# Kernel optimization log

Measured on AMD Instinct MI355X. Metric: run time of the kernel, lower is better.

The kernel has to match this reference:

```python
import jax, jax.numpy as jnp
import numpy as np

N, E, IN, H, ED, G, OUT = 50000, 800000, 128, 256, 32, 500, 16
LN_EPS = 1e-5
BN_EPS = 1e-5


def _w(key, shape, scale=0.05):
    return scale * jax.random.normal(key, shape, dtype=jnp.float32)


def setup_inputs() -> dict:
    key = jax.random.key(0)
    ks = iter(jax.random.split(key, 64))
    inp = {
        'x': jax.random.normal(next(ks), (N, IN), jnp.float32),
        'edge_index': jax.random.randint(next(ks), (2, E), 0, N, jnp.int64),
        'edge_attr': jax.random.normal(next(ks), (E, ED), jnp.float32),
        'batch': jnp.sort(jax.random.randint(next(ks), (N,), 0, G, jnp.int64)),
    }
    def conv_params(pfx, din):
        return {
            pfx + '_Wq': _w(next(ks), (din, H)), pfx + '_bq': jnp.zeros((H,), jnp.float32),
            pfx + '_Wk': _w(next(ks), (din, H)), pfx + '_bk': jnp.zeros((H,), jnp.float32),
            pfx + '_Wv': _w(next(ks), (din, H)), pfx + '_bv': jnp.zeros((H,), jnp.float32),
            pfx + '_We': _w(next(ks), (ED, H)),
            pfx + '_Ws': _w(next(ks), (din, H)), pfx + '_bs': jnp.zeros((H,), jnp.float32),
        }
    inp.update(conv_params('conv1', IN))
    inp.update({'ln1_g': jnp.ones((H,), jnp.float32), 'ln1_b': jnp.zeros((H,), jnp.float32)})
    inp.update(conv_params('conv2', H))
    inp.update({'ln2_g': jnp.ones((H,), jnp.float32), 'ln2_b': jnp.zeros((H,), jnp.float32)})
    for pfx in ('gin1', 'gin2'):
        inp.update({
            pfx + '_W1': _w(next(ks), (H, H)), pfx + '_b1': jnp.zeros((H,), jnp.float32),
            pfx + '_bng': jnp.ones((H,), jnp.float32), pfx + '_bnb': jnp.zeros((H,), jnp.float32),
            pfx + '_W2': _w(next(ks), (H, H)), pfx + '_b2': jnp.zeros((H,), jnp.float32),
        })
    inp.update({'lin_W': _w(next(ks), (H, H)), 'lin_b': jnp.zeros((H,), jnp.float32),
                'clf_W': _w(next(ks), (H, OUT)), 'clf_b': jnp.zeros((OUT,), jnp.float32)})
    return inp


def transformer_conv(x, src, dst, ea, Wq, bq, Wk, bk, Wv, bv, We, Ws, bs):
    # PyG TransformerConv, heads=1, edge_dim set, root_weight=True, beta=False
    h = Wq.shape[1]
    q = x @ Wq + bq                      # [N,H]
    e = ea @ We                          # [E,H]
    ke = (x @ Wk + bk)[src] + e          # [E,H]
    ve = (x @ Wv + bv)[src] + e          # [E,H]
    score = jnp.sum(q[dst] * ke, axis=-1) / jnp.sqrt(jnp.float32(h))  # [E]
    m = jax.ops.segment_max(score, dst, num_segments=N)
    ex = jnp.exp(score - m[dst])
    denom = jax.ops.segment_sum(ex, dst, num_segments=N)
    alpha = ex / (denom[dst] + 1e-16)
    out = jax.ops.segment_sum(alpha[:, None] * ve, dst, num_segments=N)
    return out + x @ Ws + bs


def layer_norm(x, g, b):
    mu = jnp.mean(x, axis=-1, keepdims=True)
    var = jnp.var(x, axis=-1, keepdims=True)
    return (x - mu) * jax.lax.rsqrt(var + LN_EPS) * g + b


def gin_conv(x, src, dst, W1, b1, bng, bnb, W2, b2):
    # GINConv(eps=0): mlp(x + sum_{j in N(i)} x_j); MLP = Linear-BN-ReLU-Linear
    agg = jax.ops.segment_sum(x[src], dst, num_segments=N)
    h = x + agg
    y = h @ W1 + b1
    mu = jnp.mean(y, axis=0)
    var = jnp.var(y, axis=0)
    y = (y - mu) * jax.lax.rsqrt(var + BN_EPS) * bng + bnb
    y = jax.nn.relu(y)
    return y @ W2 + b2


def reference(x, edge_index, edge_attr, batch,
              conv1_Wq, conv1_bq, conv1_Wk, conv1_bk, conv1_Wv, conv1_bv, conv1_We, conv1_Ws, conv1_bs,
              ln1_g, ln1_b,
              conv2_Wq, conv2_bq, conv2_Wk, conv2_bk, conv2_Wv, conv2_bv, conv2_We, conv2_Ws, conv2_bs,
              ln2_g, ln2_b,
              gin1_W1, gin1_b1, gin1_bng, gin1_bnb, gin1_W2, gin1_b2,
              gin2_W1, gin2_b1, gin2_bng, gin2_bnb, gin2_W2, gin2_b2,
              lin_W, lin_b, clf_W, clf_b):
    src, dst = edge_index[0], edge_index[1]
    # NodeEncoder (dropout inactive in eval)
    h = transformer_conv(x, src, dst, edge_attr, conv1_Wq, conv1_bq, conv1_Wk, conv1_bk,
                         conv1_Wv, conv1_bv, conv1_We, conv1_Ws, conv1_bs)
    h = layer_norm(jax.nn.leaky_relu(h), ln1_g, ln1_b)
    h = transformer_conv(h, src, dst, edge_attr, conv2_Wq, conv2_bq, conv2_Wk, conv2_bk,
                         conv2_Wv, conv2_bv, conv2_We, conv2_Ws, conv2_bs)
    h = layer_norm(jax.nn.leaky_relu(h), ln2_g, ln2_b)
    # GIN_Net, max_depth=2: conv -> relu -> conv
    h = gin_conv(h, src, dst, gin1_W1, gin1_b1, gin1_bng, gin1_bnb, gin1_W2, gin1_b2)
    h = jax.nn.relu(h)
    h = gin_conv(h, src, dst, gin2_W1, gin2_b1, gin2_bng, gin2_bnb, gin2_W2, gin2_b2)
    # global_add_pool + MLP head
    pooled = jax.ops.segment_sum(h, batch, num_segments=G)   # [G,H]
    z = jax.nn.relu(pooled @ lin_W + lin_b)
    return z @ clf_W + clf_b                                 # [G,OUT]
```

## Files before the change

kernel.cpp:

```cpp
#include <hip/hip_runtime.h>
#include <math.h>

#define NN 50000
#define NE 800000
#define DIN 128
#define DH 256
#define DED 32
#define NG 500
#define DOUT 16
#define SCAN_T 256

typedef __bf16 bf16_t;
typedef __bf16 bf16x4 __attribute__((ext_vector_type(4)));
typedef __bf16 bf16x8 __attribute__((ext_vector_type(8)));
typedef float f32x4 __attribute__((ext_vector_type(4)));

__device__ __forceinline__ void async_copy16(const bf16_t* g, bf16_t* l) {
  __builtin_amdgcn_global_load_lds(
      (const __attribute__((address_space(1))) void*)g,
      (__attribute__((address_space(3))) void*)l, 16, 0, 0);
}

__global__ void fill_i32(int* __restrict__ p, int v, int n) {
  int i = blockIdx.x * 256 + threadIdx.x;
  if (i < n) p[i] = v;
}
__global__ void cast_bf16x8_k(const float* __restrict__ in, bf16_t* __restrict__ o, long n8) {
  long i = (long)blockIdx.x * 256 + threadIdx.x;
  if (i >= n8) return;
  const float* sp = &in[i * 8];
  bf16x8 r;
#pragma unroll
  for (int j = 0; j < 8; ++j) r[j] = (bf16_t)sp[j];
  *(bf16x8*)&o[i * 8] = r;
}

__global__ void count_k(const int* __restrict__ dst, int* __restrict__ deg) {
  int e = blockIdx.x * 256 + threadIdx.x;
  if (e < NE) atomicAdd(&deg[dst[e]], 1);
}
__global__ void scan1(const int* __restrict__ deg, int* __restrict__ rowptr,
                      int* __restrict__ bsum, int n) {
  __shared__ int s[SCAN_T];
  int t = threadIdx.x, i = blockIdx.x * SCAN_T + t;
  int v = (i < n) ? deg[i] : 0;
  s[t] = v; __syncthreads();
  for (int off = 1; off < SCAN_T; off <<= 1) {
    int add = (t >= off) ? s[t - off] : 0;
    __syncthreads(); s[t] += add; __syncthreads();
  }
  if (i < n) rowptr[i + 1] = s[t];
  if (t == SCAN_T - 1) bsum[blockIdx.x] = s[t];
}
__global__ void scan2(const int* __restrict__ bsum, int* __restrict__ boff, int nb) {
  __shared__ int s[SCAN_T];
  int t = threadIdx.x;
  int v = (t < nb) ? bsum[t] : 0;
  s[t] = v; __syncthreads();
  for (int off = 1; off < SCAN_T; off <<= 1) {
    int add = (t >= off) ? s[t - off] : 0;
    __syncthreads(); s[t] += add; __syncthreads();
  }
  boff[t] = s[t] - v;
}
__global__ void scan3(int* __restrict__ rowptr, const int* __restrict__ boff, int n) {
  int i = blockIdx.x * 256 + threadIdx.x;
  if (i < n) rowptr[i + 1] += boff[i >> 8];
  if (i == 0) rowptr[0] = 0;
}
__global__ void scatter_k(const int* __restrict__ dst, const int* __restrict__ src,
                          const int* __restrict__ rowptr, int* __restrict__ cursor,
                          int* __restrict__ esrc, int* __restrict__ epos) {
  int e = blockIdx.x * 256 + threadIdx.x;
  if (e < NE) {
    int d = dst[e];
    int pos = rowptr[d] + atomicAdd(&cursor[d], 1);
    esrc[pos] = src[e];
    epos[e] = pos;
  }
}
__global__ void permute_ea(const int* __restrict__ epos, const float* __restrict__ ea,
                           bf16_t* __restrict__ eac) {
  long t = (long)blockIdx.x * 256 + threadIdx.x;
  if (t >= (long)NE * 4) return;
  int e = (int)(t >> 2), c8 = ((int)t & 3) * 8;
  int pos = epos[e];
  const float* sp = &ea[(size_t)e * DED + c8];
  bf16x8 o;
#pragma unroll
  for (int j = 0; j < 8; ++j) o[j] = (bf16_t)sp[j];
  *(bf16x8*)&eac[(size_t)pos * DED + c8] = o;
}

struct PackEnt { const float* src; bf16_t* dst; int K; int N; };
struct PackArgs { PackEnt e[16]; };
__global__ void pack_all(PackArgs pa) {
  PackEnt en = pa.e[blockIdx.y];
  int i = blockIdx.x * 256 + threadIdx.x;
  if (i >= en.K * en.N) return;
  int el = i & 511, f = i >> 9;
  int ntiles = en.N >> 4;
  int ks = f / ntiles, t = f - ks * ntiles;
  int lane = el >> 3, j = el & 7;
  int k = ks * 32 + (lane >> 4) * 8 + j;
  int n = t * 16 + (lane & 15);
  en.dst[i] = (bf16_t)en.src[(size_t)k * en.N + n];
}

__global__ void wqe_k(const float* __restrict__ Wq, const float* __restrict__ We,
                      const float* __restrict__ bq, float* __restrict__ Wqe,
                      float* __restrict__ bqe, int din) {
  int idx = blockIdx.x * 256 + threadIdx.x;
  if (idx < din * 32) {
    int d = idx >> 5, j = idx & 31;
    float s = 0.f;
    for (int h = 0; h < DH; ++h) s += Wq[(size_t)d * DH + h] * We[(size_t)j * DH + h];
    Wqe[idx] = s;
  }
  if (idx < 32) {
    float s = 0.f;
    for (int h = 0; h < DH; ++h) s += bq[h] * We[(size_t)idx * DH + h];
    bqe[idx] = s;
  }
}

template<int NT, int RT>
__device__ __forceinline__ void gemm_body(
    const bf16_t* __restrict__ Ab, const bf16_t* __restrict__ Wp,
    const float* __restrict__ bias, float* __restrict__ Cf, bf16_t* __restrict__ Cb,
    int M, int K, int relu, int rstride, int bx,
    float* __restrict__ psum, float* __restrict__ psq)
{
  __shared__ bf16_t Atile[RT * 2048];
  __shared__ bf16_t Btile[NT * 512];
  int tid = threadIdx.x;
  int lane = tid & 63, wv = tid >> 6;
  int base = bx * (RT * 64);
  f32x4 acc[RT][NT];
#pragma unroll
  for (int rt = 0; rt < RT; ++rt)
#pragma unroll
    for (int t = 0; t < NT; ++t) acc[rt][t] = (f32x4){0.f, 0.f, 0.f, 0.f};
  int arow = wv * (16 * RT) + (lane & 15);
  int aq = (lane >> 4) * 8;
  int nk = K >> 5;
  const int ACH = RT * 256;
  const int NCH = ACH + NT * 64;
  for (int ks = 0; ks < nk; ++ks) {
    __syncthreads();
    for (int c = tid; c < NCH; c += 256) {
      if (c < ACH) {
        int r = c >> 2, q = c & 3;
        async_copy16(Ab + (size_t)(base + r) * K + ks * 32 + q * 8, &Atile[c * 8]);
      } else {
        int cb = c - ACH;
        async_copy16(Wp + (size_t)ks * NT * 512 + cb * 8, &Btile[cb * 8]);
      }
    }
    __syncthreads();
    bf16x8 a[RT];
#pragma unroll
    for (int rt = 0; rt < RT; ++rt)
      a[rt] = *(const bf16x8*)&Atile[(arow + rt * 16) * 32 + aq];
#pragma unroll
    for (int t = 0; t < NT; ++t) {
      bf16x8 b = *(const bf16x8*)&Btile[t * 512 + lane * 8];
#pragma unroll
      for (int rt = 0; rt < RT; ++rt)
        acc[rt][t] = __builtin_amdgcn_mfma_f32_16x16x32_bf16(a[rt], b, acc[rt][t], 0, 0, 0);
    }
  }
  int col_l = lane & 15;
#pragma unroll
  for (int rt = 0; rt < RT; ++rt) {
    int rbase = base + wv * (16 * RT) + rt * 16 + (lane >> 4) * 4;
#pragma unroll
    for (int t = 0; t < NT; ++t) {
      int col = t * 16 + col_l;
      float bv = bias ? bias[col] : 0.f;
#pragma unroll
      for (int r = 0; r < 4; ++r) {
        int row = rbase + r;
        if (row >= M) continue;
        float vv = acc[rt][t][r] + bv;
        if (relu) vv = fmaxf(vv, 0.f);
        if (Cf) Cf[(size_t)row * rstride + col] = vv;
        if (Cb) Cb[(size_t)row * rstride + col] = (bf16_t)vv;
      }
    }
  }
  if (psum) {
#pragma unroll
    for (int t = 0; t < NT; ++t) {
      float sc = 0.f, sq = 0.f;
      float bv = bias[t * 16 + col_l];
#pragma unroll
      for (int rt = 0; rt < RT; ++rt) {
        int rbase = base + wv * (16 * RT) + rt * 16 + (lane >> 4) * 4;
#pragma unroll
        for (int r = 0; r < 4; ++r) {
          if (rbase + r >= M) continue;
          float vv = acc[rt][t][r] + bv;
          sc += vv; sq += vv * vv;
        }
      }
      sc += __shfl_xor(sc, 16, 64); sc += __shfl_xor(sc, 32, 64);
      sq += __shfl_xor(sq, 16, 64); sq += __shfl_xor(sq, 32, 64);
      if (lane < 16) {
        int col = t * 16 + lane;
        atomicAdd(&psum[wv * DH + col], sc);
        atomicAdd(&psq[wv * DH + col], sq);
      }
    }
  }
}

template<int NT>
__global__ __launch_bounds__(256, 3) void gemm_r1(
    const bf16_t* __restrict__ Ab, const bf16_t* __restrict__ Wp,
    const float* __restrict__ bias, float* __restrict__ Cf, bf16_t* __restrict__ Cb,
    int M, int K, int relu, int rstride, float* psum, float* psq)
{
  gemm_body<NT, 1>(Ab, Wp, bias, Cf, Cb, M, K, relu, rstride, blockIdx.x, psum, psq);
}

struct QkvsArgs { const bf16_t* w[4]; const float* bias[4]; bf16_t* outp[4]; };
__global__ __launch_bounds__(256, 3) void gemm_qkvs(
    const bf16_t* __restrict__ Ab, QkvsArgs qa, int M, int K)
{
  int which = blockIdx.y;
  gemm_body<16, 2>(Ab, qa.w[which], qa.bias[which], nullptr, qa.outp[which], M, K, 0, 1024,
                   blockIdx.x, nullptr, nullptr);
}

__global__ __launch_bounds__(256, 3) void gemm_e2n_ln(
    const bf16_t* __restrict__ Ab, const bf16_t* __restrict__ Wp,
    const bf16_t* __restrict__ AGG, const bf16_t* __restrict__ qkvs,
    const float* __restrict__ g, const float* __restrict__ b,
    bf16_t* __restrict__ out, int M)
{
  __shared__ bf16_t Atile[2048];
  __shared__ bf16_t Btile[16 * 512];
  int tid = threadIdx.x;
  int lane = tid & 63, wv = tid >> 6;
  int base = blockIdx.x * 64;
  for (int c = tid; c < 256 + 1024; c += 256) {
    if (c < 256) {
      int r = c >> 2, q2 = c & 3;
      async_copy16(Ab + (size_t)(base + r) * 32 + q2 * 8, &Atile[c * 8]);
    } else {
      int cb = c - 256;
      async_copy16(Wp + cb * 8, &Btile[cb * 8]);
    }
  }
  __syncthreads();
  bf16x8 a0 = *(const bf16x8*)&Atile[(wv * 16 + (lane & 15)) * 32 + (lane >> 4) * 8];
  f32x4 acc[16];
#pragma unroll
  for (int t = 0; t < 16; ++t) {
    bf16x8 bfr = *(const bf16x8*)&Btile[t * 512 + lane * 8];
    acc[t] = __builtin_amdgcn_mfma_f32_16x16x32_bf16(a0, bfr, (f32x4){0.f,0.f,0.f,0.f}, 0, 0, 0);
  }
  int col_l = lane & 15;
  int rbase = base + wv * 16 + (lane >> 4) * 4;
#pragma unroll
  for (int t = 0; t < 16; ++t) {
    int col = t * 16 + col_l;
#pragma unroll
    for (int r = 0; r < 4; ++r) {
      int row = rbase + r;
      float ag = 0.f, sv = 0.f;
      if (row < M) {
        ag = (float)AGG[(size_t)row * DH + col];
        sv = (float)qkvs[(size_t)row * 1024 + 768 + col];
      }
      float t1 = acc[t][r] + ag + sv;
      acc[t][r] = (t1 > 0.f) ? t1 : 0.01f * t1;
    }
  }
  float mu[4], rstd[4];
#pragma unroll
  for (int r = 0; r < 4; ++r) {
    float sum = 0.f, sq = 0.f;
#pragma unroll
    for (int t = 0; t < 16; ++t) { sum += acc[t][r]; sq += acc[t][r] * acc[t][r]; }
#pragma unroll
    for (int off = 1; off < 16; off <<= 1) {
      sum += __shfl_xor(sum, off, 16);
      sq  += __shfl_xor(sq, off, 16);
    }
    mu[r] = sum * (1.f / DH);
    float var = sq * (1.f / DH) - mu[r] * mu[r];
    rstd[r] = rsqrtf(var + 1e-5f);
  }
#pragma unroll
  for (int t = 0; t < 16; ++t) {
    int col = t * 16 + col_l;
    float gc = g[col], bc = b[col];
#pragma unroll
    for (int r = 0; r < 4; ++r) {
      int row = rbase + r;
      if (row < M)
        out[(size_t)row * DH + col] = (bf16_t)((acc[t][r] - mu[r]) * rstd[r] * gc + bc);
    }
  }
}

__global__ __launch_bounds__(256) void conv_edge_fused(
    const int* __restrict__ rowptr, const int* __restrict__ esrc,
    const bf16_t* __restrict__ qkvs, const bf16_t* __restrict__ eac,
    const float* __restrict__ QEf,
    bf16_t* __restrict__ AGGn, bf16_t* __restrict__ EAn)
{
  int l = threadIdx.x & 31;
  int half = (threadIdx.x >> 5) & 1;
  int n = blockIdx.x * 4 + (threadIdx.x >> 6);
  if (n >= NN) return;
  float q[8];
  {
    bf16x8 t = *(const bf16x8*)&qkvs[(size_t)n * 1024 + l * 8];
#pragma unroll
    for (int j = 0; j < 8; ++j) q[j] = (float)t[j];
  }
  float qe[8];
#pragma unroll
  for (int j = 0; j < 8; ++j) qe[j] = 0.f;
  if (l < 4) {
    const float* p = &QEf[(size_t)n * DED + l * 8];
#pragma unroll
    for (int j = 0; j < 8; ++j) qe[j] = p[j];
  }
  float s = 0.f;
  float acc[8], eacc[8];
#pragma unroll
  for (int j = 0; j < 8; ++j) { acc[j] = 0.f; eacc[j] = 0.f; }
  int i0 = rowptr[n], i1 = rowptr[n + 1];
  for (int wb = i0; wb < i1; wb += 32) {
    int wcnt = min(32, i1 - wb);
    int widx = (l < wcnt) ? esrc[wb + l] : 0;
    int e = 0;
    for (; e + 8 <= wcnt; e += 8) {
      int s1 = __shfl(widx, e + half, 32);
      int s2 = __shfl(widx, e + 2 + half, 32);
      int s3 = __shfl(widx, e + 4 + half, 32);
      int s4 = __shfl(widx, e + 6 + half, 32);
      const bf16_t* b1 = &qkvs[(size_t)s1 * 1024 + 256 + l * 8];
      const bf16_t* b2 = &qkvs[(size_t)s2 * 1024 + 256 + l * 8];
      const bf16_t* b3 = &qkvs[(size_t)s3 * 1024 + 256 + l * 8];
      const bf16_t* b4 = &qkvs[(size_t)s4 * 1024 + 256 + l * 8];
      bf16x8 k1 = *(const bf16x8*)b1;
      bf16x8 k2 = *(const bf16x8*)b2;
      bf16x8 k3 = *(const bf16x8*)b3;
      bf16x8 k4 = *(const bf16x8*)b4;
      bf16x8 v1 = *(const bf16x8*)(b1 + 256);
      bf16x8 v2 = *(const bf16x8*)(b2 + 256);
      bf16x8 v3 = *(const bf16x8*)(b3 + 256);
      bf16x8 v4 = *(const bf16x8*)(b4 + 256);
      bf16x8 t1 = {}, t2 = {}, t3 = {}, t4 = {};
      if (l < 4) {
        const bf16_t* ep = &eac[(size_t)(wb + e + half) * DED + l * 8];
        t1 = *(const bf16x8*)ep;
        t2 = *(const bf16x8*)(ep + 2 * DED);
        t3 = *(const bf16x8*)(ep + 4 * DED);
        t4 = *(const bf16x8*)(ep + 6 * DED);
      }
      float p1 = 0.f, p2 = 0.f, p3 = 0.f, p4 = 0.f;
#pragma unroll
      for (int j = 0; j < 8; ++j) {
        p1 = fmaf(q[j], (float)k1[j], p1);
        p2 = fmaf(q[j], (float)k2[j], p2);
        p3 = fmaf(q[j], (float)k3[j], p3);
        p4 = fmaf(q[j], (float)k4[j], p4);
      }
#pragma unroll
      for (int j = 0; j < 8; ++j) {
        p1 = fmaf(qe[j], (float)t1[j], p1);
        p2 = fmaf(qe[j], (float)t2[j], p2);
        p3 = fmaf(qe[j], (float)t3[j], p3);
        p4 = fmaf(qe[j], (float)t4[j], p4);
      }
#pragma unroll
      for (int off = 16; off > 0; off >>= 1) {
        p1 += __shfl_xor(p1, off, 32);
        p2 += __shfl_xor(p2, off, 32);
        p3 += __shfl_xor(p3, off, 32);
        p4 += __shfl_xor(p4, off, 32);
      }
      float ex1 = __expf(p1 * 0.0625f);
      float ex2 = __expf(p2 * 0.0625f);
      float ex3 = __expf(p3 * 0.0625f);
      float ex4 = __expf(p4 * 0.0625f);
      s += (ex1 + ex2) + (ex3 + ex4);
#pragma unroll
      for (int j = 0; j < 8; ++j) {
        acc[j] = fmaf(ex1, (float)v1[j], acc[j]);
        acc[j] = fmaf(ex2, (float)v2[j], acc[j]);
        acc[j] = fmaf(ex3, (float)v3[j], acc[j]);
        acc[j] = fmaf(ex4, (float)v4[j], acc[j]);
      }
#pragma unroll
      for (int j = 0; j < 8; ++j) {
        eacc[j] = fmaf(ex1, (float)t1[j], eacc[j]);
        eacc[j] = fmaf(ex2, (float)t2[j], eacc[j]);
        eacc[j] = fmaf(ex3, (float)t3[j], eacc[j]);
        eacc[j] = fmaf(ex4, (float)t4[j], eacc[j]);
      }
    }
    for (; e < wcnt; e += 2) {
      int eh = e + half;
      bool act = eh < wcnt;
      int s1 = __shfl(widx, act ? eh : e, 32);
      const bf16_t* b1 = &qkvs[(size_t)s1 * 1024 + 256 + l * 8];
      bf16x8 k1 = *(const bf16x8*)b1;
      bf16x8 v1 = *(const bf16x8*)(b1 + 256);
      bf16x8 t1 = {};
      if (act && l < 4) t1 = *(const bf16x8*)&eac[(size_t)(wb + eh) * DED + l * 8];
      float p1 = 0.f;
#pragma unroll
      for (int j = 0; j < 8; ++j) p1 = fmaf(q[j], (float)k1[j], p1);
#pragma unroll
      for (int j = 0; j < 8; ++j) p1 = fmaf(qe[j], (float)t1[j], p1);
#pragma unroll
      for (int off = 16; off > 0; off >>= 1) p1 += __shfl_xor(p1, off, 32);
      float ex1 = act ? __expf(p1 * 0.0625f) : 0.f;
      s += ex1;
#pragma unroll
      for (int j = 0; j < 8; ++j) acc[j] = fmaf(ex1, (float)v1[j], acc[j]);
#pragma unroll
      for (int j = 0; j < 8; ++j) eacc[j] = fmaf(ex1, (float)t1[j], eacc[j]);
    }
  }
  s += __shfl_xor(s, 32, 64);
#pragma unroll
  for (int j = 0; j < 8; ++j) acc[j] += __shfl_xor(acc[j], 32, 64);
#pragma unroll
  for (int j = 0; j < 8; ++j) eacc[j] += __shfl_xor(eacc[j], 32, 64);
  float inv = 1.f / (s + 1e-16f);
  if (half == 0) {
    bf16x8 o;
#pragma unroll
    for (int j = 0; j < 8; ++j) o[j] = (bf16_t)(acc[j] * inv);
    *(bf16x8*)&AGGn[(size_t)n * DH + l * 8] = o;
    if (l < 4) {
      bf16x8 eo;
#pragma unroll
      for (int j = 0; j < 8; ++j) eo[j] = (bf16_t)(eacc[j] * inv);
      *(bf16x8*)&EAn[(size_t)n * DED + l * 8] = eo;
    }
  }
}

__global__ __launch_bounds__(256) void gin_gather(
    const int* __restrict__ rowptr, const int* __restrict__ esrc,
    const bf16_t* __restrict__ h, bf16_t* __restrict__ out)
{
  int l = threadIdx.x & 31;
  int half = (threadIdx.x >> 5) & 1;
  int n = blockIdx.x * 4 + (threadIdx.x >> 6);
  if (n >= NN) return;
  size_t co = (size_t)n * DH + l * 8;
  float acc[8];
  {
    bf16x8 hv = *(const bf16x8*)&h[co];
    float w0 = (half == 0) ? 1.f : 0.f;
#pragma unroll
    for (int j = 0; j < 8; ++j) acc[j] = w0 * (float)hv[j];
  }
  int i0 = rowptr[n], i1 = rowptr[n + 1];
  for (int wb = i0; wb < i1; wb += 32) {
    int wcnt = min(32, i1 - wb);
    int widx = (l < wcnt) ? esrc[wb + l] : 0;
    int e = 0;
    for (; e + 8 <= wcnt; e += 8) {
      int s1 = __shfl(widx, e + half, 32);
      int s2 = __shfl(widx, e + 2 + half, 32);
      int s3 = __shfl(widx, e + 4 + half, 32);
      int s4 = __shfl(widx, e + 6 + half, 32);
      bf16x8 t1 = *(const bf16x8*)&h[(size_t)s1 * DH + l * 8];
      bf16x8 t2 = *(const bf16x8*)&h[(size_t)s2 * DH + l * 8];
      bf16x8 t3 = *(const bf16x8*)&h[(size_t)s3 * DH + l * 8];
      bf16x8 t4 = *(const bf16x8*)&h[(size_t)s4 * DH + l * 8];
#pragma unroll
      for (int j = 0; j < 8; ++j)
        acc[j] += ((float)t1[j] + (float)t2[j]) + ((float)t3[j] + (float)t4[j]);
    }
    for (; e < wcnt; e += 2) {
      int eh = e + half;
      bool act = eh < wcnt;
      int s1 = __shfl(widx, act ? eh : e, 32);
      bf16x8 t1 = *(const bf16x8*)&h[(size_t)s1 * DH + l * 8];
      float w = act ? 1.f : 0.f;
#pragma unroll
      for (int j = 0; j < 8; ++j) acc[j] += w * (float)t1[j];
    }
  }
#pragma unroll
  for (int j = 0; j < 8; ++j) acc[j] += __shfl_xor(acc[j], 32, 64);
  if (half == 0) {
    bf16x8 o;
#pragma unroll
    for (int j = 0; j < 8; ++j) o[j] = (bf16_t)acc[j];
    *(bf16x8*)&out[co] = o;
  }
}

__global__ void bn_final_na(const float* __restrict__ psum, const float* __restrict__ psq,
                            const float* __restrict__ bng, const float* __restrict__ bnb,
                            float* __restrict__ scale, float* __restrict__ shift) {
  int c = threadIdx.x;
  float s = 0.f, ss = 0.f;
  for (int b = 0; b < 4; ++b) { s += psum[b * DH + c]; ss += psq[b * DH + c]; }
  float mu = s * (1.f / NN);
  float var = ss * (1.f / NN) - mu * mu;
  float rstd = rsqrtf(var + 1e-5f);
  float sc = bng[c] * rstd;
  scale[c] = sc;
  shift[c] = bnb[c] - mu * sc;
}
__global__ void bn_apply_relu8(const bf16_t* __restrict__ y, const float* __restrict__ scale,
                               const float* __restrict__ shift, bf16_t* __restrict__ o, int n8) {
  int i = blockIdx.x * 256 + threadIdx.x;
  if (i >= n8) return;
  bf16x8 v = *(const bf16x8*)&y[(size_t)i * 8];
  int c = (i * 8) & (DH - 1);
  bf16x8 r;
#pragma unroll
  for (int j = 0; j < 8; ++j)
    r[j] = (bf16_t)fmaxf((float)v[j] * scale[c + j] + shift[c + j], 0.f);
  *(bf16x8*)&o[(size_t)i * 8] = r;
}

__global__ __launch_bounds__(256) void pool_sorted(
    const int* __restrict__ batch, const bf16_t* __restrict__ h, float* __restrict__ pooled)
{
  __shared__ int s0, s1;
  int g = blockIdx.x;
  if (threadIdx.x == 0) {
    int lo = 0, hi = NN;
    while (lo < hi) { int mid = (lo + hi) >> 1; if (batch[mid] < g) lo = mid + 1; else hi = mid; }
    s0 = lo;
  }
  if (threadIdx.x == 1) {
    int lo = 0, hi = NN;
    while (lo < hi) { int mid = (lo + hi) >> 1; if (batch[mid] < g + 1) lo = mid + 1; else hi = mid; }
    s1 = lo;
  }
  __syncthreads();
  int c = threadIdx.x;
  float acc = 0.f;
  for (int r = s0; r < s1; ++r) acc += (float)h[(size_t)r * DH + c];
  pooled[(size_t)g * DH + c] = acc;
}

__global__ __launch_bounds__(256) void gemm_bias_act(
    const float* __restrict__ A, const float* __restrict__ Wm,
    const float* __restrict__ bias, float* __restrict__ C,
    int M, int K, int Ncol, int act)
{
  __shared__ __align__(16) float As[16][68];
  __shared__ __align__(16) float Bs[16][68];
  int tid = threadIdx.x;
  int tx = tid & 15, ty = tid >> 4;
  int row0 = blockIdx.y * 64 + ty * 4;
  int col0 = blockIdx.x * 64 + tx * 4;
  float acc[4][4] = {{0.f}};
  for (int k0 = 0; k0 < K; k0 += 16) {
#pragma unroll
    for (int l = 0; l < 4; ++l) {
      int e = tid + l * 256;
      int r = e >> 4, kk = e & 15;
      int gr = blockIdx.y * 64 + r;
      As[kk][r] = (gr < M) ? A[(size_t)gr * K + k0 + kk] : 0.f;
    }
#pragma unroll
    for (int l = 0; l < 4; ++l) {
      int e = tid + l * 256;
      int kk = e >> 6, c = e & 63;
      int gc = blockIdx.x * 64 + c;
      Bs[kk][c] = (gc < Ncol) ? Wm[(size_t)(k0 + kk) * Ncol + gc] : 0.f;
    }
    __syncthreads();
#pragma unroll
    for (int kk = 0; kk < 16; ++kk) {
      float4 a4 = *(const float4*)&As[kk][ty * 4];
      float4 b4 = *(const float4*)&Bs[kk][tx * 4];
      float a[4] = {a4.x, a4.y, a4.z, a4.w};
      float b[4] = {b4.x, b4.y, b4.z, b4.w};
#pragma unroll
      for (int i = 0; i < 4; ++i)
#pragma unroll
        for (int j = 0; j < 4; ++j)
          acc[i][j] = fmaf(a[i], b[j], acc[i][j]);
    }
    __syncthreads();
  }
#pragma unroll
  for (int i = 0; i < 4; ++i) {
    int r = row0 + i;
    if (r >= M) continue;
#pragma unroll
    for (int j = 0; j < 4; ++j) {
      int c = col0 + j;
      if (c >= Ncol) continue;
      float val = acc[i][j];
      if (bias) val += bias[c];
      if (act == 1) val = fmaxf(val, 0.f);
      C[(size_t)r * Ncol + c] = val;
    }
  }
}

static inline void launch_filli(hipStream_t st, int* p, int v, long n) {
  fill_i32<<<dim3((unsigned)((n + 255) / 256)), dim3(256), 0, st>>>(p, v, (int)n);
}

extern "C" void kernel_launch(void* const* d_in, const int* in_sizes, int n_in,
                              void* d_out, int out_size, void* d_ws, size_t ws_size,
                              hipStream_t stream) {
  const float* x  = (const float*)d_in[0];
  const int* ei   = (const int*)d_in[1];
  const float* ea = (const float*)d_in[2];
  const int* batch = (const int*)d_in[3];
  const int* src = ei;
  const int* dst = ei + NE;

  const float* c1[9]; for (int i = 0; i < 9; ++i) c1[i] = (const float*)d_in[4 + i];
  const float* ln1g = (const float*)d_in[13]; const float* ln1b = (const float*)d_in[14];
  const float* c2[9]; for (int i = 0; i < 9; ++i) c2[i] = (const float*)d_in[15 + i];
  const float* ln2g = (const float*)d_in[24]; const float* ln2b = (const float*)d_in[25];
  const float* g1[6]; for (int i = 0; i < 6; ++i) g1[i] = (const float*)d_in[26 + i];
  const float* g2[6]; for (int i = 0; i < 6; ++i) g2[i] = (const float*)d_in[32 + i];
  const float* linW = (const float*)d_in[38]; const float* linb = (const float*)d_in[39];
  const float* clfW = (const float*)d_in[40]; const float* clfb = (const float*)d_in[41];
  float* out = (float*)d_out;

  size_t off = 0;
  auto alloc = [&](size_t bytes) -> void* {
    void* r = (char*)d_ws + off;
    off += (bytes + 255) & ~(size_t)255;
    return r;
  };
  int* deg    = (int*)alloc(NN * 4);
  int* cursor = (int*)alloc(NN * 4);
  int* rowptr = (int*)alloc((NN + 1) * 4);
  int* esrc   = (int*)alloc((size_t)NE * 4);
  int* epos   = (int*)alloc((size_t)NE * 4);
  int* bsum   = (int*)alloc(1024);
  int* boff   = (int*)alloc(1024);
  float* QEf   = (float*)alloc((size_t)NN * DED * 4);
  float* pooled = (float*)alloc((size_t)NG * DH * 4);
  float* zbuf   = (float*)alloc((size_t)NG * DH * 4);
  float* psum  = (float*)alloc(4 * DH * 4);
  float* psq   = (float*)alloc(4 * DH * 4);
  float* bnscale = (float*)alloc(DH * 4);
  float* bnshift = (float*)alloc(DH * 4);
  float* wqe_tmp1 = (float*)alloc((size_t)DIN * DED * 4);
  float* wqe_tmp2 = (float*)alloc((size_t)DH * DED * 4);
  float* bqe1 = (float*)alloc(DED * 4);
  float* bqe2 = (float*)alloc(DED * 4);
  bf16_t* qkvsb = (bf16_t*)alloc((size_t)NN * 1024 * 2);
  bf16_t* h_b = (bf16_t*)alloc((size_t)NN * DH * 2);
  bf16_t* g_b = (bf16_t*)alloc((size_t)NN * DH * 2);
  bf16_t* Yb  = (bf16_t*)alloc((size_t)NN * DH * 2);
  bf16_t* AGGb = (bf16_t*)alloc((size_t)NN * DH * 2);
  bf16_t* EAn = (bf16_t*)alloc((size_t)NN * DED * 2);
  bf16_t* xb  = (bf16_t*)alloc((size_t)NN * DIN * 2);
  bf16_t* eac = (bf16_t*)alloc((size_t)NE * DED * 2);
  bf16_t* Hb = (bf16_t*)qkvsb;
  bf16_t* pk1q = (bf16_t*)alloc(DIN * DH * 2);
  bf16_t* pk1k = (bf16_t*)alloc(DIN * DH * 2);
  bf16_t* pk1v = (bf16_t*)alloc(DIN * DH * 2);
  bf16_t* pk1s = (bf16_t*)alloc(DIN * DH * 2);
  bf16_t* pk1qe = (bf16_t*)alloc(DIN * DED * 2);
  bf16_t* pk1we = (bf16_t*)alloc(DED * DH * 2);
  bf16_t* pk2q = (bf16_t*)alloc(DH * DH * 2);
  bf16_t* pk2k = (bf16_t*)alloc(DH * DH * 2);
  bf16_t* pk2v = (bf16_t*)alloc(DH * DH * 2);
  bf16_t* pk2s = (bf16_t*)alloc(DH * DH * 2);
  bf16_t* pk2qe = (bf16_t*)alloc(DH * DED * 2);
  bf16_t* pk2we = (bf16_t*)alloc(DED * DH * 2);
  bf16_t* pkg1a = (bf16_t*)alloc(DH * DH * 2);
  bf16_t* pkg1b = (bf16_t*)alloc(DH * DH * 2);
  bf16_t* pkg2a = (bf16_t*)alloc(DH * DH * 2);
  bf16_t* pkg2b = (bf16_t*)alloc(DH * DH * 2);
  if (ws_size < off) return;

  const int GRID_M  = (NN + 127) / 128;
  const int GRID_M1 = (NN + 63) / 64;

  cast_bf16x8_k<<<dim3((unsigned)(((long)NN * DIN / 8 + 255) / 256)), dim3(256), 0, stream>>>(
      x, xb, (long)NN * DIN / 8);
  wqe_k<<<dim3((DIN * 32 + 255) / 256), dim3(256), 0, stream>>>(c1[0], c1[6], c1[1], wqe_tmp1, bqe1, DIN);
  wqe_k<<<dim3((DH * 32 + 255) / 256), dim3(256), 0, stream>>>(c2[0], c2[6], c2[1], wqe_tmp2, bqe2, DH);
  PackArgs pa;
  pa.e[0]  = {c1[0], pk1q, DIN, DH};
  pa.e[1]  = {c1[2], pk1k, DIN, DH};
  pa.e[2]  = {c1[4], pk1v, DIN, DH};
  pa.e[3]  = {c1[7], pk1s, DIN, DH};
  pa.e[4]  = {c1[6], pk1we, DED, DH};
  pa.e[5]  = {wqe_tmp1, pk1qe, DIN, DED};
  pa.e[6]  = {c2[0], pk2q, DH, DH};
  pa.e[7]  = {c2[2], pk2k, DH, DH};
  pa.e[8]  = {c2[4], pk2v, DH, DH};
  pa.e[9]  = {c2[7], pk2s, DH, DH};
  pa.e[10] = {c2[6], pk2we, DED, DH};
  pa.e[11] = {wqe_tmp2, pk2qe, DH, DED};
  pa.e[12] = {g1[0], pkg1a, DH, DH};
  pa.e[13] = {g1[4], pkg1b, DH, DH};
  pa.e[14] = {g2[0], pkg2a, DH, DH};
  pa.e[15] = {g2[4], pkg2b, DH, DH};
  pack_all<<<dim3(256, 16), dim3(256), 0, stream>>>(pa);

  const int nb1 = (NN + SCAN_T - 1) / SCAN_T;
  launch_filli(stream, deg, 0, NN);
  launch_filli(stream, cursor, 0, NN);
  count_k<<<dim3((NE + 255) / 256), dim3(256), 0, stream>>>(dst, deg);
  scan1<<<dim3(nb1), dim3(SCAN_T), 0, stream>>>(deg, rowptr, bsum, NN);
  scan2<<<dim3(1), dim3(SCAN_T), 0, stream>>>(bsum, boff, nb1);
  scan3<<<dim3(nb1), dim3(SCAN_T), 0, stream>>>(rowptr, boff, NN);
  scatter_k<<<dim3((NE + 255) / 256), dim3(256), 0, stream>>>(dst, src, rowptr, cursor, esrc, epos);
  permute_ea<<<dim3((unsigned)(((long)NE * 4 + 255) / 256)), dim3(256), 0, stream>>>(epos, ea, eac);

  auto conv = [&](const bf16_t* Ain, int K,
                  const bf16_t* pq, const bf16_t* pk, const bf16_t* pv, const bf16_t* ps,
                  const bf16_t* pqe, const bf16_t* pwe,
                  const float* const* P, const float* bqe,
                  const float* lng, const float* lnb, bf16_t* outb) {
    QkvsArgs qa;
    qa.w[0] = pq; qa.w[1] = pk; qa.w[2] = pv; qa.w[3] = ps;
    qa.bias[0] = P[1]; qa.bias[1] = P[3]; qa.bias[2] = P[5]; qa.bias[3] = P[8];
    qa.outp[0] = qkvsb + 0; qa.outp[1] = qkvsb + 256;
    qa.outp[2] = qkvsb + 512; qa.outp[3] = qkvsb + 768;
    gemm_qkvs<<<dim3(GRID_M, 4), dim3(256), 0, stream>>>(Ain, qa, NN, K);
    gemm_r1<2><<<dim3(GRID_M1), dim3(256), 0, stream>>>(
        Ain, pqe, bqe, QEf, nullptr, NN, K, 0, 32, nullptr, nullptr);
    conv_edge_fused<<<dim3((NN + 3) / 4), dim3(256), 0, stream>>>(
        rowptr, esrc, qkvsb, eac, QEf, AGGb, EAn);
    gemm_e2n_ln<<<dim3(GRID_M1), dim3(256), 0, stream>>>(
        EAn, pwe, AGGb, qkvsb, lng, lnb, outb, NN);
  };

  auto gin = [&](const bf16_t* hin, const bf16_t* pw1, const bf16_t* pw2,
                 const float* const* P, int relu_out, bf16_t* outb) {
    gin_gather<<<dim3((NN + 3) / 4), dim3(256), 0, stream>>>(rowptr, esrc, hin, g_b);
    launch_filli(stream, (int*)psum, 0, 2 * 4 * DH);
    gemm_r1<16><<<dim3(GRID_M1), dim3(256), 0, stream>>>(
        g_b, pw1, P[1], nullptr, Yb, NN, DH, 0, 256, psum, psq);
    bn_final_na<<<dim3(1), dim3(256), 0, stream>>>(psum, psq, P[2], P[3], bnscale, bnshift);
    bn_apply_relu8<<<dim3((NN * DH / 8 + 255) / 256), dim3(256), 0, stream>>>(
        Yb, bnscale, bnshift, g_b, NN * DH / 8);
    gemm_r1<16><<<dim3(GRID_M1), dim3(256), 0, stream>>>(
        g_b, pw2, P[5], nullptr, outb, NN, DH, relu_out, 256, nullptr, nullptr);
  };

  conv(xb, DIN, pk1q, pk1k, pk1v, pk1s, pk1qe, pk1we, c1, bqe1, ln1g, ln1b, h_b);
  conv(h_b, DH, pk2q, pk2k, pk2v, pk2s, pk2qe, pk2we, c2, bqe2, ln2g, ln2b, h_b);
  gin(h_b, pkg1a, pkg1b, g1, 1, h_b);
  gin(h_b, pkg2a, pkg2b, g2, 0, Hb);

  pool_sorted<<<dim3(NG), dim3(256), 0, stream>>>(batch, Hb, pooled);
  gemm_bias_act<<<dim3(4, 8), dim3(256), 0, stream>>>(pooled, linW, linb, zbuf, NG, DH, DH, 1);
  gemm_bias_act<<<dim3(1, 8), dim3(256), 0, stream>>>(zbuf, clfW, clfb, out, NG, DH, DOUT, 0);
}
```

Baseline: 1.409 ms.

## Double-buffer GEMM tiles, add nontemporal loads/stores, split fused e2n+LN kernel

The GEMM body now double-buffers its A/B LDS tiles, so the next K-step's async loads overlap the current step's MFMAs. Loads and stores across many streaming kernels switch to nontemporal builtins and use float4 vectorized reads. The fused e2n GEMM plus LayerNorm kernel is replaced by a generic GEMM writing a new bf16 E2N buffer and a separate epilogue kernel that does the leaky-ReLU and LayerNorm. The split adds an extra write and read of an N×256 intermediate, and the two fill launches are merged into one, which assumes deg and cursor sit next to each other in memory.

Measured after the change: 1.280 ms. 1.1x faster.

```diff
diff --git a/kernel.cpp b/kernel.cpp
--- a/kernel.cpp
+++ b/kernel.cpp
@@ -28,10 +28,12 @@
 __global__ void cast_bf16x8_k(const float* __restrict__ in, bf16_t* __restrict__ o, long n8) {
   long i = (long)blockIdx.x * 256 + threadIdx.x;
   if (i >= n8) return;
-  const float* sp = &in[i * 8];
+  const f32x4* sp = (const f32x4*)&in[i * 8];
+  f32x4 a = __builtin_nontemporal_load(sp);
+  f32x4 b = __builtin_nontemporal_load(sp + 1);
   bf16x8 r;
 #pragma unroll
-  for (int j = 0; j < 8; ++j) r[j] = (bf16_t)sp[j];
+  for (int j = 0; j < 4; ++j) { r[j] = (bf16_t)a[j]; r[j + 4] = (bf16_t)b[j]; }
   *(bf16x8*)&o[i * 8] = r;
 }
 
@@ -85,11 +87,13 @@
   if (t >= (long)NE * 4) return;
   int e = (int)(t >> 2), c8 = ((int)t & 3) * 8;
   int pos = epos[e];
-  const float* sp = &ea[(size_t)e * DED + c8];
+  const f32x4* sp = (const f32x4*)&ea[(size_t)e * DED + c8];
+  f32x4 a = __builtin_nontemporal_load(sp);
+  f32x4 b = __builtin_nontemporal_load(sp + 1);
   bf16x8 o;
 #pragma unroll
-  for (int j = 0; j < 8; ++j) o[j] = (bf16_t)sp[j];
-  *(bf16x8*)&eac[(size_t)pos * DED + c8] = o;
+  for (int j = 0; j < 4; ++j) { o[j] = (bf16_t)a[j]; o[j + 4] = (bf16_t)b[j]; }
+  __builtin_nontemporal_store(o, (bf16x8*)&eac[(size_t)pos * DED + c8]);
 }
 
 struct PackEnt { const float* src; bf16_t* dst; int K; int N; };
@@ -131,8 +135,10 @@
     int M, int K, int relu, int rstride, int bx,
     float* __restrict__ psum, float* __restrict__ psq)
 {
-  __shared__ bf16_t Atile[RT * 2048];
-  __shared__ bf16_t Btile[NT * 512];
+  __shared__ bf16_t Atile[2][RT * 2048];
+  __shared__ bf16_t Btile[2][NT * 512];
+  const int ACH = RT * 256;
+  const int NCH = ACH + NT * 64;
   int tid = threadIdx.x;
   int lane = tid & 63, wv = tid >> 6;
   int base = bx * (RT * 64);
@@ -144,31 +150,40 @@
   int arow = wv * (16 * RT) + (lane & 15);
   int aq = (lane >> 4) * 8;
   int nk = K >> 5;
-  const int ACH = RT * 256;
-  const int NCH = ACH + NT * 64;
-  for (int ks = 0; ks < nk; ++ks) {
-    __syncthreads();
+
+  auto stage = [&](int buf, int ks) {
     for (int c = tid; c < NCH; c += 256) {
       if (c < ACH) {
-        int r = c >> 2, q = c & 3;
-        async_copy16(Ab + (size_t)(base + r) * K + ks * 32 + q * 8, &Atile[c * 8]);
+        int r = c >> 2, qq = c & 3;
+        async_copy16(Ab + (size_t)(base + r) * K + ks * 32 + qq * 8,
+                     &Atile[buf][c * 8]);
       } else {
         int cb = c - ACH;
-        async_copy16(Wp + (size_t)ks * NT * 512 + cb * 8, &Btile[cb * 8]);
-      }
-    }
-    __syncthreads();
+        async_copy16(Wp + (size_t)ks * NT * 512 + cb * 8, &Btile[buf][cb * 8]);
+      }
+    }
+  };
+
+  stage(0, 0);
+  asm volatile("s_waitcnt vmcnt(0)" ::: "memory");
+  __builtin_amdgcn_s_barrier();
+  int cur = 0;
+  for (int ks = 0; ks < nk; ++ks) {
+    if (ks + 1 < nk) stage(cur ^ 1, ks + 1);
     bf16x8 a[RT];
 #pragma unroll
     for (int rt = 0; rt < RT; ++rt)
-      a[rt] = *(const bf16x8*)&Atile[(arow + rt * 16) * 32 + aq];
+      a[rt] = *(const bf16x8*)&Atile[cur][(arow + rt * 16) * 32 + aq];
 #pragma unroll
     for (int t = 0; t < NT; ++t) {
-      bf16x8 b = *(const bf16x8*)&Btile[t * 512 + lane * 8];
+      bf16x8 b = *(const bf16x8*)&Btile[cur][t * 512 + lane * 8];
 #pragma unroll
       for (int rt = 0; rt < RT; ++rt)
         acc[rt][t] = __builtin_amdgcn_mfma_f32_16x16x32_bf16(a[rt], b, acc[rt][t], 0, 0, 0);
     }
+    asm volatile("s_waitcnt vmcnt(0)" ::: "memory");
+    __builtin_amdgcn_s_barrier();
+    cur ^= 1;
   }
   int col_l = lane & 15;
 #pragma unroll
@@ -231,79 +246,6 @@
   int which = blockIdx.y;
   gemm_body<16, 2>(Ab, qa.w[which], qa.bias[which], nullptr, qa.outp[which], M, K, 0, 1024,
                    blockIdx.x, nullptr, nullptr);
-}
-
-__global__ __launch_bounds__(256, 3) void gemm_e2n_ln(
-    const bf16_t* __restrict__ Ab, const bf16_t* __restrict__ Wp,
-    const bf16_t* __restrict__ AGG, const bf16_t* __restrict__ qkvs,
-    const float* __restrict__ g, const float* __restrict__ b,
-    bf16_t* __restrict__ out, int M)
-{
-  __shared__ bf16_t Atile[2048];
-  __shared__ bf16_t Btile[16 * 512];
-  int tid = threadIdx.x;
-  int lane = tid & 63, wv = tid >> 6;
-  int base = blockIdx.x * 64;
-  for (int c = tid; c < 256 + 1024; c += 256) {
-    if (c < 256) {
-      int r = c >> 2, q2 = c & 3;
-      async_copy16(Ab + (size_t)(base + r) * 32 + q2 * 8, &Atile[c * 8]);
-    } else {
-      int cb = c - 256;
-      async_copy16(Wp + cb * 8, &Btile[cb * 8]);
-    }
-  }
-  __syncthreads();
-  bf16x8 a0 = *(const bf16x8*)&Atile[(wv * 16 + (lane & 15)) * 32 + (lane >> 4) * 8];
-  f32x4 acc[16];
-#pragma unroll
-  for (int t = 0; t < 16; ++t) {
-    bf16x8 bfr = *(const bf16x8*)&Btile[t * 512 + lane * 8];
-    acc[t] = __builtin_amdgcn_mfma_f32_16x16x32_bf16(a0, bfr, (f32x4){0.f,0.f,0.f,0.f}, 0, 0, 0);
-  }
-  int col_l = lane & 15;
-  int rbase = base + wv * 16 + (lane >> 4) * 4;
-#pragma unroll
-  for (int t = 0; t < 16; ++t) {
-    int col = t * 16 + col_l;
-#pragma unroll
-    for (int r = 0; r < 4; ++r) {
-      int row = rbase + r;
-      float ag = 0.f, sv = 0.f;
-      if (row < M) {
-        ag = (float)AGG[(size_t)row * DH + col];
-        sv = (float)qkvs[(size_t)row * 1024 + 768 + col];
-      }
-      float t1 = acc[t][r] + ag + sv;
-      acc[t][r] = (t1 > 0.f) ? t1 : 0.01f * t1;
-    }
-  }
-  float mu[4], rstd[4];
-#pragma unroll
-  for (int r = 0; r < 4; ++r) {
-    float sum = 0.f, sq = 0.f;
-#pragma unroll
-    for (int t = 0; t < 16; ++t) { sum += acc[t][r]; sq += acc[t][r] * acc[t][r]; }
-#pragma unroll
-    for (int off = 1; off < 16; off <<= 1) {
-      sum += __shfl_xor(sum, off, 16);
-      sq  += __shfl_xor(sq, off, 16);
-    }
-    mu[r] = sum * (1.f / DH);
-    float var = sq * (1.f / DH) - mu[r] * mu[r];
-    rstd[r] = rsqrtf(var + 1e-5f);
-  }
-#pragma unroll
-  for (int t = 0; t < 16; ++t) {
-    int col = t * 16 + col_l;
-    float gc = g[col], bc = b[col];
-#pragma unroll
-    for (int r = 0; r < 4; ++r) {
-      int row = rbase + r;
-      if (row < M)
-        out[(size_t)row * DH + col] = (bf16_t)((acc[t][r] - mu[r]) * rstd[r] * gc + bc);
-    }
-  }
 }
 
 __global__ __launch_bounds__(256) void conv_edge_fused(
@@ -318,7 +260,7 @@
   if (n >= NN) return;
   float q[8];
   {
-    bf16x8 t = *(const bf16x8*)&qkvs[(size_t)n * 1024 + l * 8];
+    bf16x8 t = __builtin_nontemporal_load((const bf16x8*)&qkvs[(size_t)n * 1024 + l * 8]);
 #pragma unroll
     for (int j = 0; j < 8; ++j) q[j] = (float)t[j];
   }
@@ -326,9 +268,11 @@
 #pragma unroll
   for (int j = 0; j < 8; ++j) qe[j] = 0.f;
   if (l < 4) {
-    const float* p = &QEf[(size_t)n * DED + l * 8];
-#pragma unroll
-    for (int j = 0; j < 8; ++j) qe[j] = p[j];
+    const f32x4* p = (const f32x4*)&QEf[(size_t)n * DED + l * 8];
+    f32x4 qa = __builtin_nontemporal_load(p);
+    f32x4 qb = __builtin_nontemporal_load(p + 1);
+#pragma unroll
+    for (int j = 0; j < 4; ++j) { qe[j] = qa[j]; qe[j + 4] = qb[j]; }
   }
   float s = 0.f;
   float acc[8], eacc[8];
@@ -359,10 +303,10 @@
       bf16x8 t1 = {}, t2 = {}, t3 = {}, t4 = {};
       if (l < 4) {
         const bf16_t* ep = &eac[(size_t)(wb + e + half) * DED + l * 8];
-        t1 = *(const bf16x8*)ep;
-        t2 = *(const bf16x8*)(ep + 2 * DED);
-        t3 = *(const bf16x8*)(ep + 4 * DED);
-        t4 = *(const bf16x8*)(ep + 6 * DED);
+        t1 = __builtin_nontemporal_load((const bf16x8*)ep);
+        t2 = __builtin_nontemporal_load((const bf16x8*)(ep + 2 * DED));
+        t3 = __builtin_nontemporal_load((const bf16x8*)(ep + 4 * DED));
+        t4 = __builtin_nontemporal_load((const bf16x8*)(ep + 6 * DED));
       }
       float p1 = 0.f, p2 = 0.f, p3 = 0.f, p4 = 0.f;
 #pragma unroll
@@ -414,7 +358,8 @@
       bf16x8 k1 = *(const bf16x8*)b1;
       bf16x8 v1 = *(const bf16x8*)(b1 + 256);
       bf16x8 t1 = {};
-      if (act && l < 4) t1 = *(const bf16x8*)&eac[(size_t)(wb + eh) * DED + l * 8];
+      if (act && l < 4)
+        t1 = __builtin_nontemporal_load((const bf16x8*)&eac[(size_t)(wb + eh) * DED + l * 8]);
       float p1 = 0.f;
 #pragma unroll
       for (int j = 0; j < 8; ++j) p1 = fmaf(q[j], (float)k1[j], p1);
@@ -440,14 +385,50 @@
     bf16x8 o;
 #pragma unroll
     for (int j = 0; j < 8; ++j) o[j] = (bf16_t)(acc[j] * inv);
-    *(bf16x8*)&AGGn[(size_t)n * DH + l * 8] = o;
+    __builtin_nontemporal_store(o, (bf16x8*)&AGGn[(size_t)n * DH + l * 8]);
     if (l < 4) {
       bf16x8 eo;
 #pragma unroll
       for (int j = 0; j < 8; ++j) eo[j] = (bf16_t)(eacc[j] * inv);
-      *(bf16x8*)&EAn[(size_t)n * DED + l * 8] = eo;
-    }
-  }
+      __builtin_nontemporal_store(eo, (bf16x8*)&EAn[(size_t)n * DED + l * 8]);
+    }
+  }
+}
+
+__global__ __launch_bounds__(256) void conv_epilogue(
+    const bf16_t* __restrict__ AGGn, const bf16_t* __restrict__ E2N,
+    const bf16_t* __restrict__ qkvs, const float* __restrict__ g,
+    const float* __restrict__ b, bf16_t* __restrict__ out)
+{
+  int wv = threadIdx.x >> 6, lane = threadIdx.x & 63;
+  int n = blockIdx.x * 4 + wv;
+  if (n >= NN) return;
+  size_t base = (size_t)n * DH + lane * 4;
+  bf16x4 a = __builtin_nontemporal_load((const bf16x4*)&AGGn[base]);
+  bf16x4 e2 = __builtin_nontemporal_load((const bf16x4*)&E2N[base]);
+  bf16x4 sv = __builtin_nontemporal_load(
+      (const bf16x4*)&qkvs[(size_t)n * 1024 + 768 + lane * 4]);
+  float v[4];
+#pragma unroll
+  for (int j = 0; j < 4; ++j) {
+    float t = (float)a[j] + (float)e2[j] + (float)sv[j];
+    v[j] = (t > 0.f) ? t : 0.01f * t;
+  }
+  float sum = v[0] + v[1] + v[2] + v[3];
+  float sq = v[0]*v[0] + v[1]*v[1] + v[2]*v[2] + v[3]*v[3];
+#pragma unroll
+  for (int off = 32; off > 0; off >>= 1) {
+    sum += __shfl_xor(sum, off, 64);
+    sq  += __shfl_xor(sq, off, 64);
+  }
+  float mu = sum * (1.f / DH);
+  float var = sq * (1.f / DH) - mu * mu;
+  float rstd = rsqrtf(var + 1e-5f);
+  bf16x4 o;
+#pragma unroll
+  for (int j = 0; j < 4; ++j)
+    o[j] = (bf16_t)((v[j] - mu) * rstd * g[lane * 4 + j] + b[lane * 4 + j]);
+  *(bf16x4*)&out[base] = o;
 }
 
 __global__ __launch_bounds__(256) void gin_gather(
@@ -500,7 +481,7 @@
     bf16x8 o;
 #pragma unroll
     for (int j = 0; j < 8; ++j) o[j] = (bf16_t)acc[j];
-    *(bf16x8*)&out[co] = o;
+    __builtin_nontemporal_store(o, (bf16x8*)&out[co]);
   }
 }
 
@@ -521,7 +502,7 @@
                                const float* __restrict__ shift, bf16_t* __restrict__ o, int n8) {
   int i = blockIdx.x * 256 + threadIdx.x;
   if (i >= n8) return;
-  bf16x8 v = *(const bf16x8*)&y[(size_t)i * 8];
+  bf16x8 v = __builtin_nontemporal_load((const bf16x8*)&y[(size_t)i * 8]);
   int c = (i * 8) & (DH - 1);
   bf16x8 r;
 #pragma unroll
@@ -548,7 +529,8 @@
   __syncthreads();
   int c = threadIdx.x;
   float acc = 0.f;
-  for (int r = s0; r < s1; ++r) acc += (float)h[(size_t)r * DH + c];
+  for (int r = s0; r < s1; ++r)
+    acc += (float)__builtin_nontemporal_load(&h[(size_t)r * DH + c]);
   pooled[(size_t)g * DH + c] = acc;
 }
 
@@ -663,6 +645,7 @@
   bf16_t* g_b = (bf16_t*)alloc((size_t)NN * DH * 2);
   bf16_t* Yb  = (bf16_t*)alloc((size_t)NN * DH * 2);
   bf16_t* AGGb = (bf16_t*)alloc((size_t)NN * DH * 2);
+  bf16_t* E2Nb = (bf16_t*)alloc((size_t)NN * DH * 2);
   bf16_t* EAn = (bf16_t*)alloc((size_t)NN * DED * 2);
   bf16_t* xb  = (bf16_t*)alloc((size_t)NN * DIN * 2);
   bf16_t* eac = (bf16_t*)alloc((size_t)NE * DED * 2);
@@ -712,8 +695,7 @@
   pack_all<<<dim3(256, 16), dim3(256), 0, stream>>>(pa);
 
   const int nb1 = (NN + SCAN_T - 1) / SCAN_T;
-  launch_filli(stream, deg, 0, NN);
-  launch_filli(stream, cursor, 0, NN);
+  launch_filli(stream, deg, 0, 2 * ((NN * 4 + 255) & ~255) / 4);
   count_k<<<dim3((NE + 255) / 256), dim3(256), 0, stream>>>(dst, deg);
   scan1<<<dim3(nb1), dim3(SCAN_T), 0, stream>>>(deg, rowptr, bsum, NN);
   scan2<<<dim3(1), dim3(SCAN_T), 0, stream>>>(bsum, boff, nb1);
@@ -736,8 +718,10 @@
         Ain, pqe, bqe, QEf, nullptr, NN, K, 0, 32, nullptr, nullptr);
     conv_edge_fused<<<dim3((NN + 3) / 4), dim3(256), 0, stream>>>(
         rowptr, esrc, qkvsb, eac, QEf, AGGb, EAn);
-    gemm_e2n_ln<<<dim3(GRID_M1), dim3(256), 0, stream>>>(
-        EAn, pwe, AGGb, qkvsb, lng, lnb, outb, NN);
+    gemm_r1<16><<<dim3(GRID_M1), dim3(256), 0, stream>>>(
+        EAn, pwe, nullptr, nullptr, E2Nb, NN, DED, 0, 256, nullptr, nullptr);
+    conv_epilogue<<<dim3((NN + 3) / 4), dim3(256), 0, stream>>>(
+        AGGb, E2Nb, qkvsb, lng, lnb, outb);
   };
 
   auto gin = [&](const bf16_t* hin, const bf16_t* pw1, const bf16_t* pw2,
```
